# Performance work log

Measured on AMD Instinct MI355X. Metric: run time of the kernel, lower is better.

## Reference

```python
import jax, jax.numpy as jnp
import numpy as np

DIM = 1024
N_HEADS = 16
DIM_FF = 4096
EPS = 1e-12


def layer_norm(x, gamma, beta):
    u = jnp.mean(x, axis=-1, keepdims=True)
    s = jnp.mean((x - u) ** 2, axis=-1, keepdims=True)
    return gamma * ((x - u) / jnp.sqrt(s + EPS)) + beta


def setup_inputs() -> dict:
    key = jax.random.key(0)
    ks = jax.random.split(key, 12)
    B, S, D, F = 2, 2048, DIM, DIM_FF
    init = lambda k, shape: (jax.random.normal(k, shape, dtype=jnp.float32) * 0.02)
    return {
        "x": jax.random.normal(ks[0], (B, S, D), dtype=jnp.float32),
        "mask": jnp.ones((B, S), dtype=jnp.int32),
        "wq": init(ks[1], (D, D)), "bq": jnp.zeros((D,), jnp.float32),
        "wk": init(ks[2], (D, D)), "bk": jnp.zeros((D,), jnp.float32),
        "wv": init(ks[3], (D, D)), "bv": jnp.zeros((D,), jnp.float32),
        "wo": init(ks[4], (D, D)), "bo": jnp.zeros((D,), jnp.float32),
        "g1": jnp.ones((D,), jnp.float32), "b1": jnp.zeros((D,), jnp.float32),
        "w1": init(ks[5], (D, F)), "bf1": jnp.zeros((F,), jnp.float32),
        "w2": init(ks[6], (F, D)), "bf2": jnp.zeros((D,), jnp.float32),
        "g2": jnp.ones((D,), jnp.float32), "b2": jnp.zeros((D,), jnp.float32),
    }


def reference(x, mask, wq, bq, wk, bk, wv, bv, wo, bo, g1, b1, w1, bf1, w2, bf2, g2, b2):
    B, S, D = x.shape
    H = N_HEADS
    W = D // H
    # QKV projections -> (B, H, S, W)
    def heads(y):
        return y.reshape(B, S, H, W).transpose(0, 2, 1, 3)
    q = heads(x @ wq + bq)
    k = heads(x @ wk + bk)
    v = heads(x @ wv + bv)
    # scaled dot-product attention with additive mask (exact module math)
    scores = jnp.einsum('bhsw,bhtw->bhst', q, k) / np.sqrt(W).astype(np.float32)
    m = mask.astype(jnp.float32)[:, None, None, :]  # (B,1,1,S)
    scores = scores - 10000.0 * (1.0 - m)
    attn = jax.nn.softmax(scores, axis=-1)
    h = jnp.einsum('bhst,bhtw->bhsw', attn, v).transpose(0, 2, 1, 3).reshape(B, S, D)
    # residual + LN1
    h = layer_norm(x + (h @ wo + bo), g1, b1)
    # position-wise FFN with exact-erf GELU, residual + LN2
    ff = jax.nn.gelu(h @ w1 + bf1, approximate=False) @ w2 + bf2
    return layer_norm(h + ff, g2, b2)
```

## Files before the change

kernel.cpp:

```cpp
#include <hip/hip_runtime.h>
#include <cstdint>
#include <cstddef>

using u16 = unsigned short;
using u32 = unsigned int;

typedef __bf16 bf16x8 __attribute__((ext_vector_type(8)));
typedef float f32x4 __attribute__((ext_vector_type(4)));

static constexpr int Bb = 2, S = 2048, D = 1024, H = 16, W = 64, F = 4096;
static constexpr int M = Bb * S;

__device__ __forceinline__ float bf2f(u16 u) {
  union { u32 i; float f; } c; c.i = ((u32)u) << 16; return c.f;
}
__device__ __forceinline__ u16 f2bf(float f) {
  union { float f; u32 i; } c; c.f = f;
  u32 i = c.i;
  u32 r = (i + 0x7fffu + ((i >> 16) & 1u)) >> 16;
  return (u16)r;
}
__device__ __forceinline__ __bf16 u2b(u16 x) {
  union { u16 u; __bf16 b; } c; c.u = x; return c.b;
}
__device__ __forceinline__ void stv(float* p, size_t i, float v) { p[i] = v; }
__device__ __forceinline__ void stv(u16* p, size_t i, float v)   { p[i] = f2bf(v); }
__device__ __forceinline__ float ldv(const float* p, size_t i) { return p[i]; }
__device__ __forceinline__ float ldv(const u16* p, size_t i)   { return bf2f(p[i]); }

__device__ __forceinline__ void async_cp16(const u16* g, u16* l) {
  __builtin_amdgcn_global_load_lds(
      (const __attribute__((address_space(1))) void*)g,
      (__attribute__((address_space(3))) void*)l, 16, 0, 0);
}

__global__ __launch_bounds__(256) void conv_x_kernel(
    const float* __restrict__ src, u16* __restrict__ dst)
{
  int i = (blockIdx.x * 256 + threadIdx.x) * 4;
  float4 v = *(const float4*)(src + i);
  u16 r[4] = { f2bf(v.x), f2bf(v.y), f2bf(v.z), f2bf(v.w) };
  *(uint2*)(dst + i) = *(const uint2*)r;
}

__global__ __launch_bounds__(256) void transpose_w_kernel(
    const float* __restrict__ src, u16* __restrict__ dst, int K, int N)
{
  __shared__ __align__(16) u16 T[64][72];
  const int tid = threadIdx.x;
  const int n0 = blockIdx.x * 64, k0 = blockIdx.y * 64;
#pragma unroll
  for (int t = 0; t < 4; t++) {
    int idx = tid + t * 256;
    int r = idx >> 4, c4 = (idx & 15) * 4;
    float4 v = *(const float4*)(src + (size_t)(k0 + r) * N + n0 + c4);
    T[c4 + 0][r] = f2bf(v.x); T[c4 + 1][r] = f2bf(v.y);
    T[c4 + 2][r] = f2bf(v.z); T[c4 + 3][r] = f2bf(v.w);
  }
  __syncthreads();
#pragma unroll
  for (int t = 0; t < 2; t++) {
    int idx = tid + t * 256;
    int r = idx >> 3, c8 = (idx & 7) * 8;
    *(uint4*)(dst + (size_t)(n0 + r) * K + k0 + c8) = *(const uint4*)(&T[r][c8]);
  }
}

template<int EPI, typename TC>
__global__ __launch_bounds__(256) void gemm_bt(
    const u16* __restrict__ A, const u16* __restrict__ BT,
    const float* __restrict__ bias, TC* __restrict__ C,
    int N, int K, float scale)
{
  __shared__ __align__(16) u16 As[128 * 32];
  __shared__ __align__(16) u16 Bs[128 * 32];
  const int tid = threadIdx.x;
  const int wave = tid >> 6, lane = tid & 63;
  const int quad = lane >> 4, l16 = lane & 15;
  const int m0 = blockIdx.y * 128, n0 = blockIdx.x * 128;
  const int wm = (wave >> 1) * 64, wn = (wave & 1) * 64;
  const int srow = lane >> 2;
  const int skoff = (lane & 3) * 8;

  f32x4 acc[4][4] = {};

  for (int k0 = 0; k0 < K; k0 += 32) {
#pragma unroll
    for (int t = 0; t < 2; t++) {
      int slot = wave * 2 + t;
      int row = slot * 16 + srow;
      const u16* ga = A  + (size_t)(m0 + row) * K + k0 + skoff;
      const u16* gb = BT + (size_t)(n0 + row) * K + k0 + skoff;
      async_cp16(ga, As + slot * 512);
      async_cp16(gb, Bs + slot * 512);
    }
    __syncthreads();

    bf16x8 af[4], bfv[4];
#pragma unroll
    for (int i = 0; i < 4; i++)
      af[i] = *(const bf16x8*)(As + (wm + i * 16 + l16) * 32 + quad * 8);
#pragma unroll
    for (int j = 0; j < 4; j++)
      bfv[j] = *(const bf16x8*)(Bs + (wn + j * 16 + l16) * 32 + quad * 8);
#pragma unroll
    for (int i = 0; i < 4; i++)
#pragma unroll
      for (int j = 0; j < 4; j++)
        acc[i][j] = __builtin_amdgcn_mfma_f32_16x16x32_bf16(af[i], bfv[j], acc[i][j], 0, 0, 0);
    __syncthreads();
  }

#pragma unroll
  for (int i = 0; i < 4; i++) {
#pragma unroll
    for (int j = 0; j < 4; j++) {
#pragma unroll
      for (int r = 0; r < 4; r++) {
        int row = m0 + wm + i * 16 + quad * 4 + r;
        int col = n0 + wn + j * 16 + l16;
        float val = acc[i][j][r] + bias[col];
        if (EPI == 1) {
          val = 0.5f * val * (1.0f + erff(val * 0.70710678118654752f));
        }
        if (EPI == 2) {
          int sel = col >> 10, c = col & 1023;
          if (sel == 0) val *= scale;
          int bb = row >> 11, ss = row & 2047;
          int hh = c >> 6,  ww = c & 63;
          u16* dst = (u16*)C + (size_t)sel * M * D;
          dst[(((size_t)(bb * H + hh) * S) + ss) * W + ww] = f2bf(val);
        } else {
          stv(C, (size_t)row * N + col, val);
        }
      }
    }
  }
}

template<typename TC>
__global__ __launch_bounds__(256) void gemm_bt64(
    const u16* __restrict__ A, const u16* __restrict__ BT,
    const float* __restrict__ bias, TC* __restrict__ C,
    int N, int K)
{
  __shared__ __align__(16) u16 As[64 * 32];
  __shared__ __align__(16) u16 Bs[64 * 32];
  const int tid = threadIdx.x;
  const int wave = tid >> 6, lane = tid & 63;
  const int quad = lane >> 4, l16 = lane & 15;
  const int m0 = blockIdx.y * 64, n0 = blockIdx.x * 64;
  const int wm = (wave >> 1) * 32, wn = (wave & 1) * 32;
  const int srow = lane >> 2;
  const int skoff = (lane & 3) * 8;

  f32x4 acc[2][2] = {};

  for (int k0 = 0; k0 < K; k0 += 32) {
    int row = wave * 16 + srow;
    async_cp16(A  + (size_t)(m0 + row) * K + k0 + skoff, As + wave * 512);
    async_cp16(BT + (size_t)(n0 + row) * K + k0 + skoff, Bs + wave * 512);
    __syncthreads();

    bf16x8 af[2], bfv[2];
#pragma unroll
    for (int i = 0; i < 2; i++)
      af[i] = *(const bf16x8*)(As + (wm + i * 16 + l16) * 32 + quad * 8);
#pragma unroll
    for (int j = 0; j < 2; j++)
      bfv[j] = *(const bf16x8*)(Bs + (wn + j * 16 + l16) * 32 + quad * 8);
#pragma unroll
    for (int i = 0; i < 2; i++)
#pragma unroll
      for (int j = 0; j < 2; j++)
        acc[i][j] = __builtin_amdgcn_mfma_f32_16x16x32_bf16(af[i], bfv[j], acc[i][j], 0, 0, 0);
    __syncthreads();
  }

#pragma unroll
  for (int i = 0; i < 2; i++) {
#pragma unroll
    for (int j = 0; j < 2; j++) {
#pragma unroll
      for (int r = 0; r < 4; r++) {
        int row = m0 + wm + i * 16 + quad * 4 + r;
        int col = n0 + wn + j * 16 + l16;
        stv(C, (size_t)row * N + col, acc[i][j][r] + bias[col]);
      }
    }
  }
}

__global__ __launch_bounds__(256) void transpose_v_kernel(
    const u16* __restrict__ v, u16* __restrict__ vt)
{
  __shared__ __align__(16) u16 T[64][72];
  const int bh = blockIdx.y, k0 = blockIdx.x * 64, tid = threadIdx.x;
#pragma unroll
  for (int it = 0; it < 2; it++) {
    int vv = tid + it * 256;
    int key = vv >> 3, w0 = (vv & 7) * 8;
    union { uint4 q; u16 e[8]; } u;
    u.q = *(const uint4*)(v + ((size_t)bh * S + k0 + key) * W + w0);
#pragma unroll
    for (int j = 0; j < 8; j++) T[w0 + j][key] = u.e[j];
  }
  __syncthreads();
#pragma unroll
  for (int it = 0; it < 2; it++) {
    int vv = tid + it * 256;
    int w = vv >> 3, koff = (vv & 7) * 8;
    *(uint4*)(vt + ((size_t)bh * W + w) * S + k0 + koff) = *(const uint4*)(&T[w][koff]);
  }
}

__global__ __launch_bounds__(256) void fattn_kernel(
    const u16* __restrict__ q, const u16* __restrict__ k,
    const u16* __restrict__ vt, const int* __restrict__ mask,
    u16* __restrict__ out)
{
  __shared__ __align__(16) u16 QP[64][72];
  __shared__ __align__(16) u16 Kl[64][72];
  __shared__ __align__(16) u16 Vl[64][72];
  __shared__ float msk[64];

  const int tid = threadIdx.x, wave = tid >> 6, lane = tid & 63;
  const int quad = lane >> 4, l16 = lane & 15;
  const int bh = blockIdx.y, b = bh >> 4, h = bh & 15;
  const int q0 = blockIdx.x * 64;
  const int w16 = wave * 16;

#pragma unroll
  for (int it = 0; it < 2; it++) {
    int vv = tid + it * 256;
    int r = vv >> 3, c0 = (vv & 7) * 8;
    *(uint4*)(&QP[r][c0]) = *(const uint4*)(q + ((size_t)bh * S + q0 + r) * W + c0);
  }
  __syncthreads();
  bf16x8 aq[2];
#pragma unroll
  for (int kc = 0; kc < 2; kc++)
    aq[kc] = *(const bf16x8*)(&QP[w16 + l16][kc * 32 + quad * 8]);

  bf16x8 ones;
  {
    u16 ov = (l16 == 0) ? (u16)0x3F80 : (u16)0;
#pragma unroll
    for (int j = 0; j < 8; j++) ones[j] = u2b(ov);
  }

  float m_run = -1e30f;
  f32x4 o_acc[4] = {};
  f32x4 l_acc = {};

  for (int kt = 0; kt < S / 64; kt++) {
    __syncthreads();
#pragma unroll
    for (int it = 0; it < 2; it++) {
      int vv = tid + it * 256;
      int r = vv >> 3, c0 = (vv & 7) * 8;
      *(uint4*)(&Kl[r][c0]) = *(const uint4*)(k  + ((size_t)bh * S + kt * 64 + r) * W + c0);
      *(uint4*)(&Vl[r][c0]) = *(const uint4*)(vt + ((size_t)bh * W + r) * S + kt * 64 + c0);
    }
    if (tid < 64) msk[tid] = -10000.0f * (1.0f - (float)mask[b * S + kt * 64 + tid]);
    __syncthreads();

    f32x4 sc[4] = {};
#pragma unroll
    for (int tn = 0; tn < 4; tn++) {
#pragma unroll
      for (int kc = 0; kc < 2; kc++) {
        bf16x8 bk = *(const bf16x8*)(&Kl[tn * 16 + l16][kc * 32 + quad * 8]);
        sc[tn] = __builtin_amdgcn_mfma_f32_16x16x32_bf16(aq[kc], bk, sc[tn], 0, 0, 0);
      }
    }
    float lmax = -1e30f;
#pragma unroll
    for (int tn = 0; tn < 4; tn++) {
      float mm = msk[tn * 16 + l16];
#pragma unroll
      for (int r = 0; r < 4; r++) {
        sc[tn][r] += mm;
        lmax = fmaxf(lmax, sc[tn][r]);
      }
    }
#pragma unroll
    for (int d = 1; d < 64; d <<= 1) lmax = fmaxf(lmax, __shfl_xor(lmax, d));
    float mnew = fmaxf(m_run, lmax);
    float alpha = __expf(m_run - mnew);
    m_run = mnew;

#pragma unroll
    for (int tn = 0; tn < 4; tn++) {
#pragma unroll
      for (int r = 0; r < 4; r++) {
        float pv = __expf(sc[tn][r] - mnew);
        o_acc[tn][r] *= alpha;
        QP[w16 + quad * 4 + r][tn * 16 + l16] = f2bf(pv);
      }
    }
#pragma unroll
    for (int r = 0; r < 4; r++) l_acc[r] *= alpha;
    __syncthreads();

#pragma unroll
    for (int kc = 0; kc < 2; kc++) {
      bf16x8 ap = *(const bf16x8*)(&QP[w16 + l16][kc * 32 + quad * 8]);
#pragma unroll
      for (int tn = 0; tn < 4; tn++) {
        bf16x8 bv = *(const bf16x8*)(&Vl[tn * 16 + l16][kc * 32 + quad * 8]);
        o_acc[tn] = __builtin_amdgcn_mfma_f32_16x16x32_bf16(ap, bv, o_acc[tn], 0, 0, 0);
      }
      l_acc = __builtin_amdgcn_mfma_f32_16x16x32_bf16(ap, ones, l_acc, 0, 0, 0);
    }
  }

#pragma unroll
  for (int r = 0; r < 4; r++) {
    float lsum = __shfl(l_acc[r], lane & 0x30);
    float inv = 1.0f / lsum;
    int sg = q0 + w16 + quad * 4 + r;
#pragma unroll
    for (int tn = 0; tn < 4; tn++) {
      out[((size_t)b * S + sg) * D + h * W + tn * 16 + l16] = f2bf(o_acc[tn][r] * inv);
    }
  }
}

template<typename TA, typename TR, typename TO>
__global__ __launch_bounds__(256) void ln_res_kernel(
    const TA* __restrict__ a, const TR* __restrict__ r,
    const float* __restrict__ g, const float* __restrict__ be,
    TO* __restrict__ out)
{
  const int row = blockIdx.x;
  const int tid = threadIdx.x;
  __shared__ float red[256];
  const TA* ap = a + (size_t)row * D;
  const TR* rp = r + (size_t)row * D;
  float hv[4];
  float lsum = 0.f;
#pragma unroll
  for (int c = 0; c < 4; c++) {
    int d = tid + c * 256;
    hv[c] = ldv(ap, d) + ldv(rp, d);
    lsum += hv[c];
  }
  red[tid] = lsum; __syncthreads();
  for (int st = 128; st > 0; st >>= 1) { if (tid < st) red[tid] += red[tid + st]; __syncthreads(); }
  float mean = red[0] * (1.0f / D);
  __syncthreads();
  float lv = 0.f;
#pragma unroll
  for (int c = 0; c < 4; c++) { float dd = hv[c] - mean; lv += dd * dd; }
  red[tid] = lv; __syncthreads();
  for (int st = 128; st > 0; st >>= 1) { if (tid < st) red[tid] += red[tid + st]; __syncthreads(); }
  float varr = red[0] * (1.0f / D);
  float inv = rsqrtf(varr + 1e-12f);
#pragma unroll
  for (int c = 0; c < 4; c++) {
    int d = tid + c * 256;
    stv(out, (size_t)row * D + d, g[d] * ((hv[c] - mean) * inv) + be[d]);
  }
}

extern "C" void kernel_launch(void* const* d_in, const int* in_sizes, int n_in,
                              void* d_out, int out_size, void* d_ws, size_t ws_size,
                              hipStream_t stream)
{
  const float* x  = (const float*)d_in[0];
  const int* mask = (const int*)d_in[1];
  const float* wq = (const float*)d_in[2];  const float* bq  = (const float*)d_in[3];
  const float* wk = (const float*)d_in[4];  const float* bk  = (const float*)d_in[5];
  const float* wv = (const float*)d_in[6];  const float* bv  = (const float*)d_in[7];
  const float* wo = (const float*)d_in[8];  const float* bo  = (const float*)d_in[9];
  const float* g1 = (const float*)d_in[10]; const float* b1  = (const float*)d_in[11];
  const float* w1 = (const float*)d_in[12]; const float* bf1 = (const float*)d_in[13];
  const float* w2 = (const float*)d_in[14]; const float* bf2 = (const float*)d_in[15];
  const float* g2 = (const float*)d_in[16]; const float* b2  = (const float*)d_in[17];

  char* ws = (char*)d_ws;
  const size_t MB = 1024 * 1024;
  u16* wqkvT = (u16*)(ws + 0 * MB);
  u16* woT   = (u16*)(ws + 6 * MB);
  u16* w1T   = (u16*)(ws + 0 * MB);
  u16* w2T   = (u16*)(ws + 0 * MB);
  u16* xb    = (u16*)(ws + 8 * MB);
  u16* vt    = (u16*)(ws + 8 * MB);
  u16* q     = (u16*)(ws + 16 * MB);
  u16* proj  = (u16*)(ws + 16 * MB);
  u16* kb    = (u16*)(ws + 24 * MB);
  u16* vb    = (u16*)(ws + 32 * MB);
  u16* attn  = (u16*)(ws + 32 * MB);
  u16* ff1   = (u16*)(ws + 8 * MB);
  float* bqkv = (float*)(ws + 40 * MB);
  u16* h1    = (u16*)(ws + 40 * MB);
  float* out = (float*)d_out;

  dim3 blk(256);

  conv_x_kernel<<<dim3(M * D / 1024), blk, 0, stream>>>(x, xb);
  transpose_w_kernel<<<dim3(16, 16), blk, 0, stream>>>(wq, wqkvT,            D, D);
  transpose_w_kernel<<<dim3(16, 16), blk, 0, stream>>>(wk, wqkvT + 1024*1024, D, D);
  transpose_w_kernel<<<dim3(16, 16), blk, 0, stream>>>(wv, wqkvT + 2048*1024, D, D);
  transpose_w_kernel<<<dim3(16, 16), blk, 0, stream>>>(wo, woT,              D, D);
  hipMemcpyAsync(bqkv,        bq, D * sizeof(float), hipMemcpyDeviceToDevice, stream);
  hipMemcpyAsync(bqkv + 1024, bk, D * sizeof(float), hipMemcpyDeviceToDevice, stream);
  hipMemcpyAsync(bqkv + 2048, bv, D * sizeof(float), hipMemcpyDeviceToDevice, stream);

  gemm_bt<2, u16><<<dim3(3072 / 128, M / 128), blk, 0, stream>>>(
      xb, wqkvT, bqkv, q, 3072, D, 0.125f);

  transpose_v_kernel<<<dim3(S / 64, Bb * H), blk, 0, stream>>>(vb, vt);
  fattn_kernel<<<dim3(S / 64, Bb * H), blk, 0, stream>>>(q, kb, vt, mask, attn);

  gemm_bt64<u16><<<dim3(D / 64, M / 64), blk, 0, stream>>>(
      attn, woT, bo, proj, D, D);
  ln_res_kernel<float, u16, u16><<<dim3(M), blk, 0, stream>>>(x, proj, g1, b1, h1);

  transpose_w_kernel<<<dim3(F / 64, D / 64), blk, 0, stream>>>(w1, w1T, D, F);
  gemm_bt<1, u16><<<dim3(F / 128, M / 128), blk, 0, stream>>>(
      h1, w1T, bf1, ff1, F, D, 1.0f);

  transpose_w_kernel<<<dim3(D / 64, F / 64), blk, 0, stream>>>(w2, w2T, F, D);
  gemm_bt64<float><<<dim3(D / 64, M / 64), blk, 0, stream>>>(
      ff1, w2T, bf2, out, D, F);
  ln_res_kernel<u16, float, float><<<dim3(M), blk, 0, stream>>>(h1, out, g2, b2, out);
}
```

Baseline: 468.2 us.

## Enlarge N=1024 GEMM tiles to 128x64 and trim flash-attention softmax overhead

The GEMM used for the output projection and the second FFN matmul now uses 128x64 block tiles instead of 64x64. Each wave computes a 64x32 sub-tile, which raises MFMA work per LDS load and halves the block count. In the attention kernel, the rescale of the running output and sum by alpha is skipped when the max did not change. One __syncthreads is dropped, relying on each wave reading back only the P rows it wrote itself. Float-to-bf16 conversion now uses the compiler cast instead of manual round-to-nearest bit arithmetic. Costs: the bigger GEMM tile uses more accumulator registers and launches fewer blocks, and the removed barrier leans on intra-wave LDS ordering.

```diff
diff --git a/kernel.cpp b/kernel.cpp
--- a/kernel.cpp
+++ b/kernel.cpp
@@ -19,6 +19,10 @@
   u32 i = c.i;
   u32 r = (i + 0x7fffu + ((i >> 16) & 1u)) >> 16;
   return (u16)r;
+}
+__device__ __forceinline__ u16 f2bf_cvt(float f) {
+  __bf16 b = (__bf16)f;
+  union { __bf16 b; u16 u; } c; c.b = b; return c.u;
 }
 __device__ __forceinline__ __bf16 u2b(u16 x) {
   union { u16 u; __bf16 b; } c; c.u = x; return c.b;
@@ -139,38 +143,45 @@
 }
 
 template<typename TC>
-__global__ __launch_bounds__(256) void gemm_bt64(
+__global__ __launch_bounds__(256) void gemm_bt_n64(
     const u16* __restrict__ A, const u16* __restrict__ BT,
     const float* __restrict__ bias, TC* __restrict__ C,
     int N, int K)
 {
-  __shared__ __align__(16) u16 As[64 * 32];
+  __shared__ __align__(16) u16 As[128 * 32];
   __shared__ __align__(16) u16 Bs[64 * 32];
   const int tid = threadIdx.x;
   const int wave = tid >> 6, lane = tid & 63;
   const int quad = lane >> 4, l16 = lane & 15;
-  const int m0 = blockIdx.y * 64, n0 = blockIdx.x * 64;
-  const int wm = (wave >> 1) * 32, wn = (wave & 1) * 32;
+  const int m0 = blockIdx.y * 128, n0 = blockIdx.x * 64;
+  const int wm = (wave >> 1) * 64, wn = (wave & 1) * 32;
   const int srow = lane >> 2;
   const int skoff = (lane & 3) * 8;
 
-  f32x4 acc[2][2] = {};
+  f32x4 acc[4][2] = {};
 
   for (int k0 = 0; k0 < K; k0 += 32) {
-    int row = wave * 16 + srow;
-    async_cp16(A  + (size_t)(m0 + row) * K + k0 + skoff, As + wave * 512);
-    async_cp16(BT + (size_t)(n0 + row) * K + k0 + skoff, Bs + wave * 512);
-    __syncthreads();
-
-    bf16x8 af[2], bfv[2];
-#pragma unroll
-    for (int i = 0; i < 2; i++)
+#pragma unroll
+    for (int t = 0; t < 2; t++) {
+      int slot = wave * 2 + t;
+      int row = slot * 16 + srow;
+      async_cp16(A + (size_t)(m0 + row) * K + k0 + skoff, As + slot * 512);
+    }
+    {
+      int row = wave * 16 + srow;
+      async_cp16(BT + (size_t)(n0 + row) * K + k0 + skoff, Bs + wave * 512);
+    }
+    __syncthreads();
+
+    bf16x8 af[4], bfv[2];
+#pragma unroll
+    for (int i = 0; i < 4; i++)
       af[i] = *(const bf16x8*)(As + (wm + i * 16 + l16) * 32 + quad * 8);
 #pragma unroll
     for (int j = 0; j < 2; j++)
       bfv[j] = *(const bf16x8*)(Bs + (wn + j * 16 + l16) * 32 + quad * 8);
 #pragma unroll
-    for (int i = 0; i < 2; i++)
+    for (int i = 0; i < 4; i++)
 #pragma unroll
       for (int j = 0; j < 2; j++)
         acc[i][j] = __builtin_amdgcn_mfma_f32_16x16x32_bf16(af[i], bfv[j], acc[i][j], 0, 0, 0);
@@ -178,7 +189,7 @@
   }
 
 #pragma unroll
-  for (int i = 0; i < 2; i++) {
+  for (int i = 0; i < 4; i++) {
 #pragma unroll
     for (int j = 0; j < 2; j++) {
 #pragma unroll
@@ -295,13 +306,17 @@
 #pragma unroll
       for (int r = 0; r < 4; r++) {
         float pv = __expf(sc[tn][r] - mnew);
-        o_acc[tn][r] *= alpha;
-        QP[w16 + quad * 4 + r][tn * 16 + l16] = f2bf(pv);
-      }
-    }
-#pragma unroll
-    for (int r = 0; r < 4; r++) l_acc[r] *= alpha;
-    __syncthreads();
+        QP[w16 + quad * 4 + r][tn * 16 + l16] = f2bf_cvt(pv);
+      }
+    }
+    if (alpha < 1.0f) {
+#pragma unroll
+      for (int tn = 0; tn < 4; tn++)
+#pragma unroll
+        for (int r = 0; r < 4; r++) o_acc[tn][r] *= alpha;
+#pragma unroll
+      for (int r = 0; r < 4; r++) l_acc[r] *= alpha;
+    }
 
 #pragma unroll
     for (int kc = 0; kc < 2; kc++) {
@@ -322,7 +337,7 @@
     int sg = q0 + w16 + quad * 4 + r;
 #pragma unroll
     for (int tn = 0; tn < 4; tn++) {
-      out[((size_t)b * S + sg) * D + h * W + tn * 16 + l16] = f2bf(o_acc[tn][r] * inv);
+      out[((size_t)b * S + sg) * D + h * W + tn * 16 + l16] = f2bf_cvt(o_acc[tn][r] * inv);
     }
   }
 }
@@ -414,7 +429,7 @@
   transpose_v_kernel<<<dim3(S / 64, Bb * H), blk, 0, stream>>>(vb, vt);
   fattn_kernel<<<dim3(S / 64, Bb * H), blk, 0, stream>>>(q, kb, vt, mask, attn);
 
-  gemm_bt64<u16><<<dim3(D / 64, M / 64), blk, 0, stream>>>(
+  gemm_bt_n64<u16><<<dim3(D / 64, M / 128), blk, 0, stream>>>(
       attn, woT, bo, proj, D, D);
   ln_res_kernel<float, u16, u16><<<dim3(M), blk, 0, stream>>>(x, proj, g1, b1, h1);
 
@@ -423,7 +438,7 @@
       h1, w1T, bf1, ff1, F, D, 1.0f);
 
   transpose_w_kernel<<<dim3(D / 64, F / 64), blk, 0, stream>>>(w2, w2T, F, D);
-  gemm_bt64<float><<<dim3(D / 64, M / 64), blk, 0, stream>>>(
+  gemm_bt_n64<float><<<dim3(D / 64, M / 128), blk, 0, stream>>>(
       ff1, w2T, bf2, out, D, F);
   ln_res_kernel<u16, float, float><<<dim3(M), blk, 0, stream>>>(h1, out, g2, b2, out);
 }
```

New measurement: 460.8 us. Within noise of the previous version (-1.6%).
